# Optimization experiments

Hardware: AMD Instinct MI355X
Metric: run time of the kernel (lower is better)

## Reference

```python
import jax, jax.numpy as jnp
import numpy as np

E = 128
H = 4
D = E // H  # head dim = 32
NEG = -1e9


def setup_inputs() -> dict:
    key = jax.random.key(0)
    ks = jax.random.split(key, 4)
    B, N = 8, 2048
    x = jax.random.normal(ks[0], (B, N, E), dtype=jnp.float32)
    adj = jax.random.randint(ks[1], (B, N, N), 0, 2, dtype=jnp.int32)
    # nn.MultiheadAttention params: packed in_proj (3E,E) + out_proj (E,E)
    in_proj_w = jax.random.normal(ks[2], (3 * E, E), dtype=jnp.float32) * (1.0 / np.sqrt(E))
    in_proj_b = jnp.zeros((3 * E,), dtype=jnp.float32)
    out_w = jax.random.normal(ks[3], (E, E), dtype=jnp.float32) * (1.0 / np.sqrt(E))
    out_b = jnp.zeros((E,), dtype=jnp.float32)
    return {"x": x, "adj": adj, "in_proj_w": in_proj_w, "in_proj_b": in_proj_b,
            "out_w": out_w, "out_b": out_b}


def reference(x, adj, in_proj_w, in_proj_b, out_w, out_b):
    B, N, _ = x.shape
    # additive mask from FIRST batch element only (as in the torch module)
    mask = jnp.where(adj[0] == 0, jnp.float32(NEG), jnp.float32(0.0))  # (N,N)
    # packed QKV projection: x @ W^T + b
    qkv = x @ in_proj_w.T + in_proj_b  # (B,N,3E)
    q, k, v = jnp.split(qkv, 3, axis=-1)
    # (B,N,E) -> (B,H,N,D)
    def heads(t):
        return t.reshape(B, N, H, D).transpose(0, 2, 1, 3)
    q, k, v = heads(q), heads(k), heads(v)
    scores = jnp.einsum('bhnd,bhmd->bhnm', q, k) / jnp.sqrt(jnp.float32(D))
    scores = scores + mask[None, None]  # broadcast shared mask
    attn = jax.nn.softmax(scores, axis=-1)
    out = jnp.einsum('bhnm,bhmd->bhnd', attn, v)  # (B,H,N,D)
    out = out.transpose(0, 2, 1, 3).reshape(B, N, E)
    return out @ out_w.T + out_b
```

## Files before the change

### kernel.cpp

```cpp
#include <hip/hip_runtime.h>


#define EDIM 128
#define SCALE2 0.25503483f
#define COFF  -5.7707801f

typedef unsigned int uint32;
typedef float f32x4 __attribute__((ext_vector_type(4)));
typedef short s16x8 __attribute__((ext_vector_type(8)));
typedef _Float16 f16x2 __attribute__((ext_vector_type(2)));
typedef _Float16 f16x4 __attribute__((ext_vector_type(4)));
typedef _Float16 f16x8 __attribute__((ext_vector_type(8)));
typedef __fp16 g16x2 __attribute__((ext_vector_type(2)));

__device__ inline float bf2f(ushort u) { return __uint_as_float(((uint32)u) << 16); }
__device__ inline ushort f2bf(float f) {
  uint32 u = __float_as_uint(f);
  u += 0x7fffu + ((u >> 16) & 1u);
  return (ushort)(u >> 16);
}
__device__ inline f16x2 pkrtz(float a, float b) {
  g16x2 t = __builtin_amdgcn_cvt_pkrtz(a, b);
  return __builtin_bit_cast(f16x2, t);
}
__device__ inline float fexp2(float x) {
#if __has_builtin(__builtin_amdgcn_exp2f)
  return __builtin_amdgcn_exp2f(x);
#else
  return __exp2f(x);
#endif
}

__device__ inline f32x4 mfma32(s16x8 a, s16x8 b, f32x4 c) {
  return __builtin_amdgcn_mfma_f32_16x16x32_bf16(a, b, c, 0, 0, 0);
}
__device__ inline f32x4 mfma32h(f16x8 a, f16x8 b, f32x4 c) {
  return __builtin_amdgcn_mfma_f32_16x16x32_f16(a, b, c, 0, 0, 0);
}

#if __has_builtin(__builtin_amdgcn_global_load_lds)
#define HAVE_GLL 1
__device__ inline void gll16(const void* g, void* l) {
  __builtin_amdgcn_global_load_lds(
      (const __attribute__((address_space(1))) unsigned int*)g,
      (__attribute__((address_space(3))) unsigned int*)l, 16, 0, 0);
}
#else
#define HAVE_GLL 0
#endif

__device__ inline int sniff_fp32(const ushort* __restrict__ xus) {
  int lane = threadIdx.x & 63, cnt = 0;
#pragma unroll
  for (int i = 0; i < 4; i++) {
    ushort v = xus[2 * (lane * 4 + i)];
    int ex = (v >> 7) & 0xFF;
    cnt += (ex >= 100 && ex <= 140) ? 1 : 0;
  }
#pragma unroll
  for (int s = 1; s < 64; s <<= 1) cnt += __shfl_xor(cnt, s);
  return cnt < 128;
}

__device__ inline s16x8 load8(const void* p, size_t e, int fp32) {
  if (fp32) {
    const float* f = (const float*)p + e;
    float4 lo = *(const float4*)f;
    float4 hi = *(const float4*)(f + 4);
    s16x8 r;
    r[0] = (short)f2bf(lo.x); r[1] = (short)f2bf(lo.y);
    r[2] = (short)f2bf(lo.z); r[3] = (short)f2bf(lo.w);
    r[4] = (short)f2bf(hi.x); r[5] = (short)f2bf(hi.y);
    r[6] = (short)f2bf(hi.z); r[7] = (short)f2bf(hi.w);
    return r;
  }
  return *(const s16x8*)((const ushort*)p + e);
}
__device__ inline float loads(const void* p, size_t e, int fp32) {
  return fp32 ? ((const float*)p)[e] : bf2f(((const ushort*)p)[e]);
}

__global__ __launch_bounds__(256) void k_mask(const int4* __restrict__ adj4,
                                              uint32* __restrict__ mb) {
  int g = blockIdx.x * 256 + threadIdx.x;
  int4 v = adj4[g];
  int lane = threadIdx.x & 63;
  uint32 nib = (v.x != 0 ? 1u : 0u) | (v.y != 0 ? 2u : 0u) |
               (v.z != 0 ? 4u : 0u) | (v.w != 0 ? 8u : 0u);
  uint32 w = nib << (4 * (lane & 7));
  w |= __shfl_xor(w, 1);
  w |= __shfl_xor(w, 2);
  w |= __shfl_xor(w, 4);
  if ((lane & 7) == 0) mb[g >> 3] = w;
}

__global__ __launch_bounds__(256) void k_qkv(const void* __restrict__ x,
                                             const void* __restrict__ w,
                                             const void* __restrict__ bias,
                                             ushort* __restrict__ Qg,
                                             ushort* __restrict__ Kg,
                                             _Float16* __restrict__ Vth) {
  const int fp32 = sniff_fp32((const ushort*)x);
  const int tid = threadIdx.x;
  const int wave = tid >> 6, lane = tid & 63, L = lane & 15, quad = lane >> 4;
  const int mt = blockIdx.x * 64 + wave * 16;
  const int jt0 = blockIdx.y * 8;

  s16x8 a[4];
#pragma unroll
  for (int ks = 0; ks < 4; ks++)
    a[ks] = load8(x, (size_t)(mt + L) * EDIM + ks * 32 + quad * 8, fp32);

  const int bidx = mt >> 11;
  const int npos0 = (mt & 2047) + quad * 4;

  for (int jj = 0; jj < 8; jj++) {
    int jt = jt0 + jj;
    f32x4 acc = {0.f, 0.f, 0.f, 0.f};
#pragma unroll
    for (int ks = 0; ks < 4; ks++) {
      s16x8 bf = load8(w, (size_t)(jt * 16 + L) * EDIM + ks * 32 + quad * 8, fp32);
      acc = mfma32(a[ks], bf, acc);
    }
    int j = jt * 16 + L;
    float badd = loads(bias, j, fp32);
    int jm = j & 127;
    int h = jm >> 5, d = jm & 31;
    int bh = bidx * 4 + h;
    int ch = npos0 >> 7, kk = npos0 & 127;
    if (jt < 8) {
#pragma unroll
      for (int r = 0; r < 4; r++)
        Qg[(size_t)bh * 65536 + (size_t)(npos0 + r) * 32 + d] = f2bf((acc[r] + badd) * SCALE2);
    } else if (jt < 16) {
      int sub = kk >> 5, k32 = kk & 31, t = k32 >> 3, r8 = k32 & 7;
      int slot0 = sub * 32 + ((r8 >> 2) << 4) + t * 4;
      size_t kb = (size_t)bh * 65536 + (size_t)ch * 4096;
#pragma unroll
      for (int r = 0; r < 4; r++)
        Kg[kb + (size_t)(slot0 + r) * 32 + (((d >> 3) ^ r) << 3) + (d & 7)] =
            f2bf(acc[r] + badd);
    } else {
      int g = kk >> 3, e0 = kk & 7;
      f16x2 h0 = pkrtz(acc[0] + badd, acc[1] + badd);
      f16x2 h1 = pkrtz(acc[2] + badd, acc[3] + badd);
      f16x4 pk; pk[0] = h0[0]; pk[1] = h0[1]; pk[2] = h1[0]; pk[3] = h1[1];
      *(f16x4*)(Vth + (size_t)bh * 65536 + (size_t)ch * 4096 + d * 128 +
                (g ^ (d & 7)) * 8 + e0) = pk;
    }
  }
}

__global__ __launch_bounds__(128) void k_attn(const ushort* __restrict__ Qg,
                                              const ushort* __restrict__ Kg,
                                              const _Float16* __restrict__ Vth,
                                              const uint32* __restrict__ mb,
                                              const ushort* __restrict__ xus,
                                              ushort* Oglob, ushort* Oa) {
  __shared__ ushort Klds[128 * 32];
  __shared__ ushort Vlds[32 * 128];

  const int fp32 = sniff_fp32(xus);
  ushort* O = fp32 ? Oa : Oglob;

  const int tid = threadIdx.x;
  const int wv = tid >> 6, lane = tid & 63, L = lane & 15, quad = lane >> 4;
  const int bh = blockIdx.x >> 5;
  const int q0 = (blockIdx.x & 31) * 64 + wv * 32;
  const int qgA = q0 + L, qgB = q0 + 16 + L;

  const ushort* Qb = Qg + (size_t)bh * 65536;
  s16x8 qfA = *(const s16x8*)(Qb + (size_t)qgA * 32 + quad * 8);
  s16x8 qfB = *(const s16x8*)(Qb + (size_t)qgB * 32 + quad * 8);

  f32x4 OA0 = {0,0,0,0}, OA1 = {0,0,0,0}, OB0 = {0,0,0,0}, OB1 = {0,0,0,0};
  f32x4 LA = {0,0,0,0}, LB = {0,0,0,0};
  f16x8 ones;
#pragma unroll
  for (int i = 0; i < 8; i++) ones[i] = (_Float16)1.0f;

  const char* Kg8 = (const char*)(Kg + (size_t)bh * 65536);
  const char* Vg8 = (const char*)(Vth + (size_t)bh * 65536);
  const int g0 = quad ^ (L & 3);

  for (int c = 0; c < 16; c++) {
    __syncthreads();
#if HAVE_GLL
#pragma unroll
    for (int j = 0; j < 4; j++) {
      int off = (wv + 2 * j) * 1024;
      gll16(Kg8 + (size_t)c * 8192 + off + lane * 16, (char*)Klds + off);
      gll16(Vg8 + (size_t)c * 8192 + off + lane * 16, (char*)Vlds + off);
    }
#else
#pragma unroll
    for (int r = 0; r < 4; r++) {
      int idx = r * 128 + tid;
      *(s16x8*)((char*)Klds + idx * 16) = *(const s16x8*)(Kg8 + (size_t)c * 8192 + idx * 16);
      *(s16x8*)((char*)Vlds + idx * 16) = *(const s16x8*)(Vg8 + (size_t)c * 8192 + idx * 16);
    }
#endif
    __syncthreads();

    uint4 mA = *(const uint4*)(mb + (size_t)qgA * 64 + c * 4);
    uint4 mB = *(const uint4*)(mb + (size_t)qgB * 64 + c * 4);
    uint32 mAw[4] = {mA.x, mA.y, mA.z, mA.w};
    uint32 mBw[4] = {mB.x, mB.y, mB.z, mB.w};

#pragma unroll
    for (int sub = 0; sub < 4; sub++) {
      const f32x4 Zc = {COFF, COFF, COFF, COFF};
      s16x8 kf0 = *(const s16x8*)&Klds[(sub * 32 + L) * 32 + g0 * 8];
      s16x8 kf1 = *(const s16x8*)&Klds[(sub * 32 + 16 + L) * 32 + g0 * 8];
      f32x4 sA0 = mfma32(kf0, qfA, Zc), sA1 = mfma32(kf1, qfA, Zc);
      f32x4 sB0 = mfma32(kf0, qfB, Zc), sB1 = mfma32(kf1, qfB, Zc);

      uint32 mwqA = mAw[sub] >> (quad * 8);
      uint32 mwqB = mBw[sub] >> (quad * 8);
      union { f16x8 v; f16x2 h[4]; } pA, pB;
      float a0 = ((mwqA >> 0) & 1u) ? fexp2(sA0[0]) : 0.f;
      float a1 = ((mwqA >> 1) & 1u) ? fexp2(sA0[1]) : 0.f;
      float a2 = ((mwqA >> 2) & 1u) ? fexp2(sA0[2]) : 0.f;
      float a3 = ((mwqA >> 3) & 1u) ? fexp2(sA0[3]) : 0.f;
      float a4 = ((mwqA >> 4) & 1u) ? fexp2(sA1[0]) : 0.f;
      float a5 = ((mwqA >> 5) & 1u) ? fexp2(sA1[1]) : 0.f;
      float a6 = ((mwqA >> 6) & 1u) ? fexp2(sA1[2]) : 0.f;
      float a7 = ((mwqA >> 7) & 1u) ? fexp2(sA1[3]) : 0.f;
      pA.h[0] = pkrtz(a0, a1); pA.h[1] = pkrtz(a2, a3);
      pA.h[2] = pkrtz(a4, a5); pA.h[3] = pkrtz(a6, a7);
      float b0 = ((mwqB >> 0) & 1u) ? fexp2(sB0[0]) : 0.f;
      float b1 = ((mwqB >> 1) & 1u) ? fexp2(sB0[1]) : 0.f;
      float b2 = ((mwqB >> 2) & 1u) ? fexp2(sB0[2]) : 0.f;
      float b3 = ((mwqB >> 3) & 1u) ? fexp2(sB0[3]) : 0.f;
      float b4 = ((mwqB >> 4) & 1u) ? fexp2(sB1[0]) : 0.f;
      float b5 = ((mwqB >> 5) & 1u) ? fexp2(sB1[1]) : 0.f;
      float b6 = ((mwqB >> 6) & 1u) ? fexp2(sB1[2]) : 0.f;
      float b7 = ((mwqB >> 7) & 1u) ? fexp2(sB1[3]) : 0.f;
      pB.h[0] = pkrtz(b0, b1); pB.h[1] = pkrtz(b2, b3);
      pB.h[2] = pkrtz(b4, b5); pB.h[3] = pkrtz(b6, b7);

      int g = (sub * 4 + quad) ^ (L & 7);
      f16x8 vf0 = *(const f16x8*)&Vlds[L * 128 + g * 8];
      f16x8 vf1 = *(const f16x8*)&Vlds[(16 + L) * 128 + g * 8];
      OA0 = mfma32h(vf0, pA.v, OA0);  OA1 = mfma32h(vf1, pA.v, OA1);
      OB0 = mfma32h(vf0, pB.v, OB0);  OB1 = mfma32h(vf1, pB.v, OB1);
      LA  = mfma32h(ones, pA.v, LA);  LB  = mfma32h(ones, pB.v, LB);
    }
  }

  int b = bh >> 2, h = bh & 3;
  {
    float rn = 1.0f / LA[0];
    size_t ob = ((size_t)(b * 2048 + qgA)) * 128 + h * 32 + quad * 4;
    ushort4 p0, p1;
    p0.x = f2bf(OA0[0] * rn); p0.y = f2bf(OA0[1] * rn);
    p0.z = f2bf(OA0[2] * rn); p0.w = f2bf(OA0[3] * rn);
    p1.x = f2bf(OA1[0] * rn); p1.y = f2bf(OA1[1] * rn);
    p1.z = f2bf(OA1[2] * rn); p1.w = f2bf(OA1[3] * rn);
    *(ushort4*)(O + ob) = p0; *(ushort4*)(O + ob + 16) = p1;
  }
  {
    float rn = 1.0f / LB[0];
    size_t ob = ((size_t)(b * 2048 + qgB)) * 128 + h * 32 + quad * 4;
    ushort4 p0, p1;
    p0.x = f2bf(OB0[0] * rn); p0.y = f2bf(OB0[1] * rn);
    p0.z = f2bf(OB0[2] * rn); p0.w = f2bf(OB0[3] * rn);
    p1.x = f2bf(OB1[0] * rn); p1.y = f2bf(OB1[1] * rn);
    p1.z = f2bf(OB1[2] * rn); p1.w = f2bf(OB1[3] * rn);
    *(ushort4*)(O + ob) = p0; *(ushort4*)(O + ob + 16) = p1;
  }
}

__global__ __launch_bounds__(256) void k_proj(void* outp, const ushort* Oa,
                                              const void* w, const void* bias,
                                              const ushort* __restrict__ xus) {
  const int fp32 = sniff_fp32(xus);
  const ushort* src = fp32 ? Oa : (const ushort*)outp;
  const int tid = threadIdx.x;
  const int wave = tid >> 6, lane = tid & 63, L = lane & 15, quad = lane >> 4;
  const int mt = blockIdx.x * 64 + wave * 16;

  s16x8 a[4];
#pragma unroll
  for (int ks = 0; ks < 4; ks++)
    a[ks] = *(const s16x8*)(src + (size_t)(mt + L) * EDIM + ks * 32 + quad * 8);

  for (int jt = 0; jt < 8; jt++) {
    f32x4 acc = {0.f, 0.f, 0.f, 0.f};
#pragma unroll
    for (int ks = 0; ks < 4; ks++) {
      s16x8 bf = load8(w, (size_t)(jt * 16 + L) * EDIM + ks * 32 + quad * 8, fp32);
      acc = mfma32(a[ks], bf, acc);
    }
    float badd = loads(bias, jt * 16 + L, fp32);
#pragma unroll
    for (int r = 0; r < 4; r++) {
      size_t idx = (size_t)(mt + quad * 4 + r) * EDIM + jt * 16 + L;
      if (fp32) ((float*)outp)[idx] = acc[r] + badd;
      else      ((ushort*)outp)[idx] = f2bf(acc[r] + badd);
    }
  }
}

extern "C" void kernel_launch(void* const* d_in, const int* in_sizes, int n_in,
                              void* d_out, int out_size, void* d_ws, size_t ws_size,
                              hipStream_t stream) {
  const void* x   = d_in[0];
  const int*  adj = (const int*)d_in[1];
  const void* ipw = d_in[2];
  const void* ipb = d_in[3];
  const void* ow  = d_in[4];
  const void* ob  = d_in[5];

  char* ws = (char*)d_ws;
  ushort*   Qg  = (ushort*)(ws);
  ushort*   Kg  = (ushort*)(ws + ((size_t)4 << 20));
  _Float16* Vth = (_Float16*)(ws + ((size_t)8 << 20));
  uint32*   mb  = (uint32*)(ws + ((size_t)12 << 20));
  ushort*   Oa  = (ushort*)(ws + ((size_t)13 << 20));

  hipLaunchKernelGGL(k_mask, dim3(4096), dim3(256), 0, stream,
                     (const int4*)adj, mb);
  hipLaunchKernelGGL(k_qkv, dim3(256, 3), dim3(256), 0, stream, x, ipw, ipb,
                     Qg, Kg, Vth);
  hipLaunchKernelGGL(k_attn, dim3(1024), dim3(128), 0, stream, Qg, Kg, Vth, mb,
                     (const ushort*)x, (ushort*)d_out, Oa);
  hipLaunchKernelGGL(k_proj, dim3(256), dim3(256), 0, stream, d_out, Oa, ow, ob,
                     (const ushort*)x);
}
```

Before: 277.5 us.

## Double-buffer K/V tiles in attention and enlarge blocks to four waves

The attention kernel now keeps two LDS buffers for K and V. It prefetches the next 128-key chunk while the current one is computed, which drops one barrier per iteration. Blocks grow from 2 to 4 waves (128 queries each) with half as many blocks, so each staged K/V tile serves more queries. The fp32-to-bf16 conversion also switches to a cheaper add-and-permute pack that rounds half-up instead of to nearest-even. In exchange, LDS use per block doubles, which may limit occupancy, and rounding changes slightly.

After: 272.4 us. About the same (-1.8%).

```diff
diff --git a/kernel.cpp b/kernel.cpp
--- a/kernel.cpp
+++ b/kernel.cpp
@@ -19,6 +19,11 @@
   u += 0x7fffu + ((u >> 16) & 1u);
   return (ushort)(u >> 16);
 }
+__device__ inline uint32 packbf(float a, float b) {
+  uint32 ua = __float_as_uint(a) + 0x8000u;
+  uint32 ub = __float_as_uint(b) + 0x8000u;
+  return __builtin_amdgcn_perm(ub, ua, 0x07060302u);
+}
 __device__ inline f16x2 pkrtz(float a, float b) {
   g16x2 t = __builtin_amdgcn_cvt_pkrtz(a, b);
   return __builtin_bit_cast(f16x2, t);
@@ -67,12 +72,12 @@
     const float* f = (const float*)p + e;
     float4 lo = *(const float4*)f;
     float4 hi = *(const float4*)(f + 4);
-    s16x8 r;
-    r[0] = (short)f2bf(lo.x); r[1] = (short)f2bf(lo.y);
-    r[2] = (short)f2bf(lo.z); r[3] = (short)f2bf(lo.w);
-    r[4] = (short)f2bf(hi.x); r[5] = (short)f2bf(hi.y);
-    r[6] = (short)f2bf(hi.z); r[7] = (short)f2bf(hi.w);
-    return r;
+    union { s16x8 s; uint32 u[4]; } r;
+    r.u[0] = packbf(lo.x, lo.y);
+    r.u[1] = packbf(lo.z, lo.w);
+    r.u[2] = packbf(hi.x, hi.y);
+    r.u[3] = packbf(hi.z, hi.w);
+    return r.s;
   }
   return *(const s16x8*)((const ushort*)p + e);
 }
@@ -151,22 +156,22 @@
   }
 }
 
-__global__ __launch_bounds__(128) void k_attn(const ushort* __restrict__ Qg,
+__global__ __launch_bounds__(256) void k_attn(const ushort* __restrict__ Qg,
                                               const ushort* __restrict__ Kg,
                                               const _Float16* __restrict__ Vth,
                                               const uint32* __restrict__ mb,
                                               const ushort* __restrict__ xus,
                                               ushort* Oglob, ushort* Oa) {
-  __shared__ ushort Klds[128 * 32];
-  __shared__ ushort Vlds[32 * 128];
+  __shared__ ushort Klds[2][128 * 32];
+  __shared__ ushort Vlds[2][32 * 128];
 
   const int fp32 = sniff_fp32(xus);
   ushort* O = fp32 ? Oa : Oglob;
 
   const int tid = threadIdx.x;
   const int wv = tid >> 6, lane = tid & 63, L = lane & 15, quad = lane >> 4;
-  const int bh = blockIdx.x >> 5;
-  const int q0 = (blockIdx.x & 31) * 64 + wv * 32;
+  const int bh = blockIdx.x >> 4;
+  const int q0 = (blockIdx.x & 15) * 128 + wv * 32;
   const int qgA = q0 + L, qgB = q0 + 16 + L;
 
   const ushort* Qb = Qg + (size_t)bh * 65536;
@@ -183,24 +188,44 @@
   const char* Vg8 = (const char*)(Vth + (size_t)bh * 65536);
   const int g0 = quad ^ (L & 3);
 
+#define STAGE(c, p)                                                          \
+  do {                                                                       \
+    _Pragma("unroll")                                                        \
+    for (int j = 0; j < 2; j++) {                                            \
+      int off = (wv + 4 * j) * 1024;                                         \
+      gll16(Kg8 + (size_t)(c) * 8192 + off + lane * 16, (char*)Klds[p] + off);\
+      gll16(Vg8 + (size_t)(c) * 8192 + off + lane * 16, (char*)Vlds[p] + off);\
+    }                                                                        \
+  } while (0)
+
+#if HAVE_GLL
+  STAGE(0, 0);
+#else
+#pragma unroll
+  for (int r = 0; r < 2; r++) {
+    int idx = r * 256 + tid;
+    *(s16x8*)((char*)Klds[0] + idx * 16) = *(const s16x8*)(Kg8 + idx * 16);
+    *(s16x8*)((char*)Vlds[0] + idx * 16) = *(const s16x8*)(Vg8 + idx * 16);
+  }
+#endif
+
   for (int c = 0; c < 16; c++) {
+    const int p = c & 1;
     __syncthreads();
 #if HAVE_GLL
-#pragma unroll
-    for (int j = 0; j < 4; j++) {
-      int off = (wv + 2 * j) * 1024;
-      gll16(Kg8 + (size_t)c * 8192 + off + lane * 16, (char*)Klds + off);
-      gll16(Vg8 + (size_t)c * 8192 + off + lane * 16, (char*)Vlds + off);
-    }
+    if (c + 1 < 16) STAGE(c + 1, 1 - p);
 #else
-#pragma unroll
-    for (int r = 0; r < 4; r++) {
-      int idx = r * 128 + tid;
-      *(s16x8*)((char*)Klds + idx * 16) = *(const s16x8*)(Kg8 + (size_t)c * 8192 + idx * 16);
-      *(s16x8*)((char*)Vlds + idx * 16) = *(const s16x8*)(Vg8 + (size_t)c * 8192 + idx * 16);
+    if (c + 1 < 16) {
+#pragma unroll
+      for (int r = 0; r < 2; r++) {
+        int idx = r * 256 + tid;
+        *(s16x8*)((char*)Klds[1 - p] + idx * 16) =
+            *(const s16x8*)(Kg8 + (size_t)(c + 1) * 8192 + idx * 16);
+        *(s16x8*)((char*)Vlds[1 - p] + idx * 16) =
+            *(const s16x8*)(Vg8 + (size_t)(c + 1) * 8192 + idx * 16);
+      }
     }
 #endif
-    __syncthreads();
 
     uint4 mA = *(const uint4*)(mb + (size_t)qgA * 64 + c * 4);
     uint4 mB = *(const uint4*)(mb + (size_t)qgB * 64 + c * 4);
@@ -210,8 +235,8 @@
 #pragma unroll
     for (int sub = 0; sub < 4; sub++) {
       const f32x4 Zc = {COFF, COFF, COFF, COFF};
-      s16x8 kf0 = *(const s16x8*)&Klds[(sub * 32 + L) * 32 + g0 * 8];
-      s16x8 kf1 = *(const s16x8*)&Klds[(sub * 32 + 16 + L) * 32 + g0 * 8];
+      s16x8 kf0 = *(const s16x8*)&Klds[p][(sub * 32 + L) * 32 + g0 * 8];
+      s16x8 kf1 = *(const s16x8*)&Klds[p][(sub * 32 + 16 + L) * 32 + g0 * 8];
       f32x4 sA0 = mfma32(kf0, qfA, Zc), sA1 = mfma32(kf1, qfA, Zc);
       f32x4 sB0 = mfma32(kf0, qfB, Zc), sB1 = mfma32(kf1, qfB, Zc);
 
@@ -240,8 +265,8 @@
       pB.h[2] = pkrtz(b4, b5); pB.h[3] = pkrtz(b6, b7);
 
       int g = (sub * 4 + quad) ^ (L & 7);
-      f16x8 vf0 = *(const f16x8*)&Vlds[L * 128 + g * 8];
-      f16x8 vf1 = *(const f16x8*)&Vlds[(16 + L) * 128 + g * 8];
+      f16x8 vf0 = *(const f16x8*)&Vlds[p][L * 128 + g * 8];
+      f16x8 vf1 = *(const f16x8*)&Vlds[p][(16 + L) * 128 + g * 8];
       OA0 = mfma32h(vf0, pA.v, OA0);  OA1 = mfma32h(vf1, pA.v, OA1);
       OB0 = mfma32h(vf0, pB.v, OB0);  OB1 = mfma32h(vf1, pB.v, OB1);
       LA  = mfma32h(ones, pA.v, LA);  LB  = mfma32h(ones, pB.v, LB);
@@ -323,7 +348,7 @@
                      (const int4*)adj, mb);
   hipLaunchKernelGGL(k_qkv, dim3(256, 3), dim3(256), 0, stream, x, ipw, ipb,
                      Qg, Kg, Vth);
-  hipLaunchKernelGGL(k_attn, dim3(1024), dim3(128), 0, stream, Qg, Kg, Vth, mb,
+  hipLaunchKernelGGL(k_attn, dim3(512), dim3(256), 0, stream, Qg, Kg, Vth, mb,
                      (const ushort*)x, (ushort*)d_out, Oa);
   hipLaunchKernelGGL(k_proj, dim3(256), dim3(256), 0, stream, d_out, Oa, ow, ob,
                      (const ushort*)x);
```
